# Kernel tuning notes

Measured on AMD Instinct MI355X. Metric: run time of the kernel, lower is better.

The kernel has to match this reference:

```python
import jax, jax.numpy as jnp
import numpy as np

N_MEM = 8
B = 64
D_K = 256
D_V = 256


def setup_inputs() -> dict:
    key0 = jax.random.key(0)
    ks = jax.random.split(key0, 7)
    INIT_SCALE = 0.01
    return {
        "states": jax.random.normal(ks[0], (N_MEM, B, D_K, D_V), dtype=jnp.float32) * INIT_SCALE,
        "key": jax.random.normal(ks[1], (B, D_K), dtype=jnp.float32),
        "value": jax.random.normal(ks[2], (B, D_V), dtype=jnp.float32),
        "alpha": jax.random.uniform(ks[3], (B, 1), dtype=jnp.float32),
        "rho": jax.random.uniform(ks[4], (B, N_MEM), dtype=jnp.float32),
        "lam": jax.random.uniform(ks[5], (B, N_MEM), dtype=jnp.float32),
        "query": jax.random.normal(ks[6], (B, D_K), dtype=jnp.float32),
    }


def reference(states, key, value, alpha, rho, lam, query):
    # One MOM step: update every memory slot, then read every slot.
    # update: M_i = lam[:, i] * M_i + (rho[:, i] * alpha) * (k outer v)
    outer = jnp.einsum("bk,bv->bkv", key, value)              # [B, Dk, Dv]
    lam_s = lam.T[:, :, None, None]                            # [N, B, 1, 1]
    write_s = (rho * alpha).T[:, :, None, None]                # [N, B, 1, 1]
    new_states = lam_s * states + write_s * outer[None]        # [N, B, Dk, Dv]
    # read: r_i = q^T M_i  -> [N, B, Dv]
    readouts = jnp.einsum("bk,nbkv->nbv", query, new_states)
    return new_states, readouts
```

## Files before the change

kernel.cpp:

```cpp
#include <hip/hip_runtime.h>

#define N_MEM 8
#define BSZ   64
#define DK    256
#define DV    256

typedef float f32x4 __attribute__((ext_vector_type(4)));

__global__ __launch_bounds__(256) void mom_kernel_fine(
    const float* __restrict__ states,
    const float* __restrict__ key,
    const float* __restrict__ value,
    const float* __restrict__ alpha,
    const float* __restrict__ rho,
    const float* __restrict__ lam,
    const float* __restrict__ query,
    float* __restrict__ out_states,
    float* __restrict__ out_read)
{
    const int bid4  = blockIdx.x;
    const int group = bid4 >> 2;
    const int chunk = bid4 & 3;
    const int n     = group >> 6;
    const int b     = group & 63;
    const int t     = threadIdx.x;

    __shared__ float s_key[64];
    __shared__ float s_q[64];
    __shared__ f32x4 s_val4[DV / 4];
    __shared__ f32x4 s_red[256];

    if (t < 64) {
        const int kg = chunk * 64 + t;
        s_key[t] = key[b * DK + kg];
        s_q[t]   = query[b * DK + kg];
    } else if (t < 128) {
        const int v4 = t - 64;
        s_val4[v4] = reinterpret_cast<const f32x4*>(value + (size_t)b * DV)[v4];
    }
    const float lam_s = lam[b * N_MEM + n];
    const float w_s   = rho[b * N_MEM + n] * alpha[b];
    __syncthreads();

    const int   v4  = t & 63;
    const f32x4 val = s_val4[v4];
    const int   k0  = t >> 6;

    const size_t base = (size_t)group * (DK * DV) + (size_t)chunk * (64 * DV);
    const f32x4* __restrict__ sp = reinterpret_cast<const f32x4*>(states + base);
    f32x4*       __restrict__ op = reinterpret_cast<f32x4*>(out_states + base);

    f32x4 racc = (f32x4)(0.f);

#pragma unroll
    for (int half = 0; half < 2; ++half) {
        f32x4 s[8];
#pragma unroll
        for (int j = 0; j < 8; ++j)
            s[j] = sp[t + (half * 8 + j) * 256];

        float kw8[8], qv8[8];
#pragma unroll
        for (int j = 0; j < 8; ++j) {
            const int it = half * 8 + j;
            kw8[j] = w_s * s_key[k0 + it * 4];
            qv8[j] = s_q[k0 + it * 4];
        }

#pragma unroll
        for (int j = 0; j < 8; ++j) {
            const int it = half * 8 + j;
            const f32x4 ns = lam_s * s[j] + kw8[j] * val;
            __builtin_nontemporal_store(ns, &op[t + it * 256]);
            racc += qv8[j] * ns;
        }
    }

    s_red[t] = racc;
    __syncthreads();
    if (t < 64) {
        f32x4 acc = s_red[t];
#pragma unroll
        for (int g = 1; g < 4; ++g)
            acc += s_red[t + g * 64];
        float* dst = out_read + (size_t)group * DV + t * 4;
        atomicAdd(dst + 0, acc.x);
        atomicAdd(dst + 1, acc.y);
        atomicAdd(dst + 2, acc.z);
        atomicAdd(dst + 3, acc.w);
    }
}

extern "C" void kernel_launch(void* const* d_in, const int* in_sizes, int n_in,
                              void* d_out, int out_size, void* d_ws, size_t ws_size,
                              hipStream_t stream) {
    const float* states = (const float*)d_in[0];
    const float* key    = (const float*)d_in[1];
    const float* value  = (const float*)d_in[2];
    const float* alpha  = (const float*)d_in[3];
    const float* rho    = (const float*)d_in[4];
    const float* lam    = (const float*)d_in[5];
    const float* query  = (const float*)d_in[6];

    float* out_states = (float*)d_out;
    float* out_read   = out_states + (size_t)N_MEM * BSZ * DK * DV;

    hipMemsetAsync(out_read, 0, (size_t)N_MEM * BSZ * DV * sizeof(float), stream);

    mom_kernel_fine<<<dim3(2048), dim3(256), 0, stream>>>(
        states, key, value, alpha, rho, lam, query, out_states, out_read);
}
```

Before: 51.18 us.

## Split work by value-column stripes to drop atomics and memset

Each block now owns a 64-column stripe of one state matrix across all 256 k rows, instead of a 64-row chunk across all columns. The full readout for that stripe is reduced inside the block and written with a plain vector store, so the separate memset launch and global atomic adds go away. The cost is a less contiguous access pattern: each group of 16 threads reads a 256-byte segment per row with a 1 KB row stride, rather than fully contiguous rows.

```diff
diff --git a/kernel.cpp b/kernel.cpp
--- a/kernel.cpp
+++ b/kernel.cpp
@@ -7,7 +7,7 @@
 
 typedef float f32x4 __attribute__((ext_vector_type(4)));
 
-__global__ __launch_bounds__(256) void mom_kernel_fine(
+__global__ __launch_bounds__(256) void mom_kernel_vstripe(
     const float* __restrict__ states,
     const float* __restrict__ key,
     const float* __restrict__ value,
@@ -18,37 +18,33 @@
     float* __restrict__ out_states,
     float* __restrict__ out_read)
 {
-    const int bid4  = blockIdx.x;
-    const int group = bid4 >> 2;
-    const int chunk = bid4 & 3;
-    const int n     = group >> 6;
-    const int b     = group & 63;
-    const int t     = threadIdx.x;
+    const int bid    = blockIdx.x;
+    const int group  = bid >> 2;
+    const int vchunk = bid & 3;
+    const int n      = group >> 6;
+    const int b      = group & 63;
+    const int t      = threadIdx.x;
 
-    __shared__ float s_key[64];
-    __shared__ float s_q[64];
-    __shared__ f32x4 s_val4[DV / 4];
+    __shared__ float s_key[DK];
+    __shared__ float s_q[DK];
+    __shared__ f32x4 s_val4[16];
     __shared__ f32x4 s_red[256];
 
-    if (t < 64) {
-        const int kg = chunk * 64 + t;
-        s_key[t] = key[b * DK + kg];
-        s_q[t]   = query[b * DK + kg];
-    } else if (t < 128) {
-        const int v4 = t - 64;
-        s_val4[v4] = reinterpret_cast<const f32x4*>(value + (size_t)b * DV)[v4];
-    }
+    s_key[t] = key[b * DK + t];
+    s_q[t]   = query[b * DK + t];
+    if (t < 16)
+        s_val4[t] = reinterpret_cast<const f32x4*>(value + (size_t)b * DV + vchunk * 64)[t];
     const float lam_s = lam[b * N_MEM + n];
     const float w_s   = rho[b * N_MEM + n] * alpha[b];
     __syncthreads();
 
-    const int   v4  = t & 63;
-    const f32x4 val = s_val4[v4];
-    const int   k0  = t >> 6;
+    const f32x4 val = s_val4[t & 15];
+    const int   kr  = t >> 4;
 
-    const size_t base = (size_t)group * (DK * DV) + (size_t)chunk * (64 * DV);
-    const f32x4* __restrict__ sp = reinterpret_cast<const f32x4*>(states + base);
-    f32x4*       __restrict__ op = reinterpret_cast<f32x4*>(out_states + base);
+    const size_t C = (size_t)group * (DK * DV / 4) + vchunk * 16 + (t & 15)
+                   + (size_t)kr * 64;
+    const f32x4* __restrict__ sp = reinterpret_cast<const f32x4*>(states) + C;
+    f32x4*       __restrict__ op = reinterpret_cast<f32x4*>(out_states) + C;
 
     f32x4 racc = (f32x4)(0.f);
 
@@ -57,37 +53,32 @@
         f32x4 s[8];
 #pragma unroll
         for (int j = 0; j < 8; ++j)
-            s[j] = sp[t + (half * 8 + j) * 256];
+            s[j] = sp[(half * 8 + j) * 1024];
 
         float kw8[8], qv8[8];
 #pragma unroll
         for (int j = 0; j < 8; ++j) {
-            const int it = half * 8 + j;
-            kw8[j] = w_s * s_key[k0 + it * 4];
-            qv8[j] = s_q[k0 + it * 4];
+            const int k = kr + (half * 8 + j) * 16;
+            kw8[j] = w_s * s_key[k];
+            qv8[j] = s_q[k];
         }
 
 #pragma unroll
         for (int j = 0; j < 8; ++j) {
-            const int it = half * 8 + j;
             const f32x4 ns = lam_s * s[j] + kw8[j] * val;
-            __builtin_nontemporal_store(ns, &op[t + it * 256]);
+            __builtin_nontemporal_store(ns, &op[(half * 8 + j) * 1024]);
             racc += qv8[j] * ns;
         }
     }
 
     s_red[t] = racc;
     __syncthreads();
-    if (t < 64) {
+    if (t < 16) {
         f32x4 acc = s_red[t];
 #pragma unroll
-        for (int g = 1; g < 4; ++g)
-            acc += s_red[t + g * 64];
-        float* dst = out_read + (size_t)group * DV + t * 4;
-        atomicAdd(dst + 0, acc.x);
-        atomicAdd(dst + 1, acc.y);
-        atomicAdd(dst + 2, acc.z);
-        atomicAdd(dst + 3, acc.w);
+        for (int g = 1; g < 16; ++g)
+            acc += s_red[t + g * 16];
+        reinterpret_cast<f32x4*>(out_read + (size_t)group * DV + vchunk * 64)[t] = acc;
     }
 }
 
@@ -105,8 +96,6 @@
     float* out_states = (float*)d_out;
     float* out_read   = out_states + (size_t)N_MEM * BSZ * DK * DV;
 
-    hipMemsetAsync(out_read, 0, (size_t)N_MEM * BSZ * DV * sizeof(float), stream);
-
-    mom_kernel_fine<<<dim3(2048), dim3(256), 0, stream>>>(
+    mom_kernel_vstripe<<<dim3(N_MEM * BSZ * 4), dim3(256), 0, stream>>>(
         states, key, value, alpha, rho, lam, query, out_states, out_read);
 }
```

Measured after the change: 44.99 us. 1.14x faster.
